# Kernel optimization log

Measured on AMD Instinct MI355X. Metric: run time of the kernel, lower is better.

Reference implementation:

```python
import jax, jax.numpy as jnp
import numpy as np

RES = 192      # resolution
RANK = 8       # low-rank
FD = 32        # feature_dim
NFPD = 32      # num_features_per_dim = round(32768**(1/3))
RADIUS = 1.3
NI = 128       # n_intersections
STEP = 0.0352  # step_size
B = 2048       # rays


def setup_inputs():
    key = jax.random.key(0)
    ks = jax.random.split(key, 12)
    ro = jax.random.normal(ks[0], (B, 3), dtype=jnp.float32)
    ro = ro / jnp.linalg.norm(ro, axis=-1, keepdims=True) * 2.5  # origins outside the cube
    rd = -ro + 0.1 * jax.random.normal(ks[1], (B, 3), dtype=jnp.float32)
    rd = rd / jnp.linalg.norm(rd, axis=-1, keepdims=True)        # roughly toward origin
    def nrm(k, shape, std):
        return std * jax.random.normal(k, shape, dtype=jnp.float32)
    return {
        "rays_o": ro, "rays_d": rd,
        "Gxy": nrm(ks[2], (RES, RES, 3, RANK), 0.1),
        "Gxz": nrm(ks[3], (RES, RES, 3, RANK), 0.1),
        "Gyz": nrm(ks[4], (RES, RES, 3, RANK), 0.1),
        "F_grid": nrm(ks[5], (NFPD, NFPD, NFPD, FD), 0.05),
        "sW0": nrm(ks[6], (FD, 128), FD ** -0.5),
        "sW1": nrm(ks[7], (128, 128), 128 ** -0.5),
        "sW2": nrm(ks[8], (128, 16), 128 ** -0.5),
        "cW0": nrm(ks[9], (31, 64), 31 ** -0.5),
        "cW1": nrm(ks[10], (64, 64), 64 ** -0.5),
        "cW2": nrm(ks[11], (64, 3), 64 ** -0.5),
    }


def trilinear(vol, coords):
    # vol: [D,H,W,C]; coords: [N,3] as (x,y,z) in [-1,1]; x indexes W (last spatial dim)
    # matches torch grid_sample(align_corners=True, mode='bilinear', padding_mode='border')
    D, H, W, C = vol.shape
    def prep(c, size):
        idx = jnp.clip((c + 1.0) * 0.5 * (size - 1), 0.0, size - 1.0)  # border clamp
        i0 = jnp.clip(jnp.floor(idx).astype(jnp.int32), 0, size - 2)
        return i0, i0 + 1, idx - i0
    x0, x1, wx = prep(coords[:, 0], W)
    y0, y1, wy = prep(coords[:, 1], H)
    z0, z1, wz = prep(coords[:, 2], D)
    wx = wx[:, None]; wy = wy[:, None]; wz = wz[:, None]
    def g(zi, yi, xi):
        return vol[zi, yi, xi]  # [N,C]
    c00 = g(z0, y0, x0) * (1 - wx) + g(z0, y0, x1) * wx
    c01 = g(z0, y1, x0) * (1 - wx) + g(z0, y1, x1) * wx
    c10 = g(z1, y0, x0) * (1 - wx) + g(z1, y0, x1) * wx
    c11 = g(z1, y1, x0) * (1 - wx) + g(z1, y1, x1) * wx
    c0 = c00 * (1 - wy) + c01 * wy
    c1 = c10 * (1 - wy) + c11 * wy
    return c0 * (1 - wz) + c1 * wz


def sh16(d):
    # tcnn SphericalHarmonics degree 4 on directions (input (d+1)/2 is unmapped back to d internally)
    x, y, z = d[:, 0], d[:, 1], d[:, 2]
    x2, y2, z2 = x * x, y * y, z * z
    return jnp.stack([
        jnp.full_like(x, 0.28209479177387814),
        -0.48860251190291987 * y,
        0.48860251190291987 * z,
        -0.48860251190291987 * x,
        1.0925484305920792 * x * y,
        -1.0925484305920792 * y * z,
        0.94617469575755997 * z2 - 0.31539156525251999,
        -1.0925484305920792 * x * z,
        0.54627421529603959 * (x2 - y2),
        0.59004358992664352 * y * (-3.0 * x2 + y2),
        2.8906114426405538 * x * y * z,
        0.45704579946446572 * y * (1.0 - 5.0 * z2),
        0.3731763325901154 * z * (5.0 * z2 - 3.0),
        0.45704579946446572 * x * (1.0 - 5.0 * z2),
        1.445305721320277 * z * (x2 - y2),
        0.59004358992664352 * x * (-x2 + 3.0 * y2),
    ], axis=-1)


def _forward(rays_o, rays_d, Gxy, Gxz, Gyz, F_grid, sW0, sW1, sW2, cW0, cW1, cW2):
    b = rays_o.shape[0]
    # --- get_intersections: ray/AABB [-R,R]^3, uniform marching ---
    d = jnp.where(jnp.abs(rays_d) < 1e-9, 1e-9, rays_d)
    t1 = (-RADIUS - rays_o) / d
    t2 = (RADIUS - rays_o) / d
    tmin = jnp.max(jnp.minimum(t1, t2), axis=-1)
    tmax = jnp.min(jnp.maximum(t1, t2), axis=-1)
    near = jnp.maximum(tmin, 0.0)
    ts = near[:, None] + jnp.arange(NI + 1, dtype=jnp.float32) * STEP  # intersections [B,NI+1]
    tmid = 0.5 * (ts[:, :-1] + ts[:, 1:])                              # [B,NI]
    pts = rays_o[:, None, :] + tmid[..., None] * rays_d[:, None, :]    # [B,NI,3]
    mask = (jnp.all(jnp.abs(pts) <= RADIUS, axis=-1)
            & (tmid <= tmax[:, None]) & (tmax > tmin)[:, None])        # [B,NI]
    rdn = rays_d / jnp.linalg.norm(rays_d, axis=-1, keepdims=True)
    # coordinate chain of forward + eval_pts nets out to pts/RADIUS in [-1,1]
    p = ((pts / RADIUS + 1.0) * RES / 2.0) * 2.0 / RES - 1.0
    pf = p.reshape(-1, 3)
    # --- densify low-rank tri-plane grid: sum_r Gxy*Gxz*Gyz -> [RES,RES,RES,3] ---
    grid = jnp.zeros((RES, RES, RES, 3), dtype=Gxy.dtype)
    for r in range(RANK):  # fixed small rank; avoids a [RES^3,3,RANK] intermediate
        grid = grid + (Gxy[:, :, None, :, r] * Gxz[:, None, :, :, r] * Gyz[None, :, :, :, r])
    # --- eval_pts: grid_sample -> hash-feature grid_sample -> MLPs ---
    Gvals = trilinear(grid, pf)            # [N,3]
    Fvals = trilinear(F_grid, Gvals)       # [N,FD]
    h = jax.nn.relu(Fvals @ sW0)
    h = jax.nn.relu(h @ sW1)
    out16 = h @ sW2                        # [N,16]
    sigma = out16[:, 0].reshape(b, NI)
    sigma = jax.nn.relu(jnp.where(mask, sigma, 0.0))
    rdn_pts = jnp.broadcast_to(rdn[:, None, :], (b, NI, 3)).reshape(-1, 3)
    ci = jnp.concatenate([sh16(rdn_pts), out16[:, 1:]], axis=-1)  # [N,31]
    c = jax.nn.relu(ci @ cW0)
    c = jax.nn.relu(c @ cW1)
    color = (c @ cW2).reshape(b, NI, 3)
    color = jnp.where(mask[..., None], color, 0.0)
    # --- sigma2alpha + shrgb2rgb (white background) ---
    dists = ts[:, 1:] - ts[:, :-1]         # |rdn| == 1
    alpha = 1.0 - jnp.exp(-sigma * dists)
    T = jnp.cumprod(1.0 - alpha + 1e-10, axis=-1)
    T = jnp.concatenate([jnp.ones_like(T[:, :1]), T[:, :-1]], axis=-1)  # exclusive
    w = alpha * T                          # abs_light [B,NI]
    rgb = jax.nn.sigmoid(color)
    acc = jnp.sum(w, axis=-1)
    return jnp.sum(w[..., None] * rgb, axis=1) + (1.0 - acc)[..., None]  # [B,3]


def reference(rays_o, rays_d, Gxy, Gxz, Gyz, F_grid, sW0, sW1, sW2, cW0, cW1, cW2):
    return _forward(rays_o, rays_d, Gxy, Gxz, Gyz, F_grid, sW0, sW1, sW2, cW0, cW1, cW2)
```

## Files before the change

kernel.cpp:

```cpp
#include <hip/hip_runtime.h>
#include <math.h>

#define RES 192
#define RANK 8
#define NI 128
#define LW 136

typedef __attribute__((ext_vector_type(8))) _Float16 h8;
typedef __attribute__((ext_vector_type(2))) _Float16 h2f;
typedef __attribute__((ext_vector_type(4))) float floatx4;

#define OFF_SW0 0
#define OFF_SW1 4096
#define OFF_SW2 20480
#define OFF_CW0 22528
#define OFF_CW1 24576
#define OFF_CW2 28672
#define PACK_TOTAL 29696

#define TRI_CELLS (RES*RES)
#define TRI_TOTAL (3*TRI_CELLS*24)
#define FG_TOTAL  (32*32*32*32)
#define PREP_TOTAL (PACK_TOTAL + TRI_TOTAL + FG_TOTAL)

__device__ __forceinline__ void prep_idx(float c, int size, int& i0, float& f){
    float idx = (c + 1.0f)*0.5f*(float)(size-1);
    idx = fminf(fmaxf(idx, 0.0f), (float)(size-1));
    int ii = (int)idx;
    if (ii > size-2) ii = size-2;
    i0 = ii;
    f = idx - (float)ii;
}

__device__ __forceinline__ float wred64(float v){
    #pragma unroll
    for (int o=32;o>0;o>>=1) v += __shfl_down(v, o, 64);
    return v;
}

__device__ __forceinline__ h8 shx1(h8 v){
    union { h8 h; int i[4]; } u; u.h = v;
    #pragma unroll
    for (int k=0;k<4;k++) u.i[k] = __shfl_xor(u.i[k], 1, 64);
    return u.h;
}

__global__ void __launch_bounds__(256) prep_all(
    const float* __restrict__ sW0, const float* __restrict__ sW1,
    const float* __restrict__ sW2, const float* __restrict__ cW0,
    const float* __restrict__ cW1, const float* __restrict__ cW2,
    const float* __restrict__ Gxy, const float* __restrict__ Gxz,
    const float* __restrict__ Gyz, const float* __restrict__ F_grid,
    _Float16* __restrict__ Wp, _Float16* __restrict__ Gp, _Float16* __restrict__ Fg)
{
    int e = blockIdx.x*256 + threadIdx.x;
    if (e < PACK_TOTAL){
        const float* src; int K, N, ksteps, base;
        if      (e < OFF_SW1){ src=sW0; K=32;  N=128; ksteps=1; base=OFF_SW0; }
        else if (e < OFF_SW2){ src=sW1; K=128; N=128; ksteps=4; base=OFF_SW1; }
        else if (e < OFF_CW0){ src=sW2; K=128; N=16;  ksteps=4; base=OFF_SW2; }
        else if (e < OFF_CW1){ src=cW0; K=31;  N=64;  ksteps=1; base=OFF_CW0; }
        else if (e < OFF_CW2){ src=cW1; K=64;  N=64;  ksteps=2; base=OFF_CW1; }
        else                 { src=cW2; K=64;  N=3;   ksteps=2; base=OFF_CW2; }
        int i = e - base;
        int j = i & 7, lane = (i>>3)&63, t = i>>9;
        int ks = t % ksteps, nt = t / ksteps;
        int k = ks*32 + (lane>>4)*8 + j;
        int n = nt*16 + (lane&15);
        float v = (k < K && n < N) ? src[k*N + n] : 0.0f;
        Wp[e] = (_Float16)v;
        return;
    }
    int e2 = e - PACK_TOTAL;
    if (e2 < TRI_TOTAL){
        int p    = e2 / (TRI_CELLS*24);
        int rem  = e2 - p*(TRI_CELLS*24);
        int cell = rem / 24;
        int c    = rem - cell*24;
        const float* src = (p==0) ? Gxy : (p==1) ? Gxz : Gyz;
        Gp[((size_t)(p*TRI_CELLS + cell))*32 + c] = (_Float16)src[(size_t)cell*24 + c];
        return;
    }
    int e3 = e2 - TRI_TOTAL;
    Fg[e3] = (_Float16)F_grid[e3];
}

__launch_bounds__(256, 4)
__global__ void nerf_fused(
    const float* __restrict__ rays_o, const float* __restrict__ rays_d,
    const _Float16* __restrict__ Gp, const _Float16* __restrict__ Fg,
    const _Float16* __restrict__ Wp, float* __restrict__ out)
{
    __shared__ _Float16 buf[128*LW];
    __shared__ float sigmaArr[128];
    __shared__ float rgbArr[128*3];
    __shared__ float wtot[2];
    __shared__ float partial[8];

    const int tid  = threadIdx.x;
    const int lane = tid & 63;
    const int wv   = tid >> 6;
    const int ray  = blockIdx.x;

    const int rowbase = wv*32;
    const int col  = lane & 15;
    const int quad = lane >> 4;
    const int ar0  = rowbase + col;
    const int ar1  = ar0 + 16;

    const float ox = rays_o[ray*3+0], oy = rays_o[ray*3+1], oz = rays_o[ray*3+2];
    const float dx = rays_d[ray*3+0], dy = rays_d[ray*3+1], dz = rays_d[ray*3+2];

    float sdx = (fabsf(dx) < 1e-9f) ? 1e-9f : dx;
    float sdy = (fabsf(dy) < 1e-9f) ? 1e-9f : dy;
    float sdz = (fabsf(dz) < 1e-9f) ? 1e-9f : dz;
    float t1x = (-1.3f - ox)/sdx, t2x = (1.3f - ox)/sdx;
    float t1y = (-1.3f - oy)/sdy, t2y = (1.3f - oy)/sdy;
    float t1z = (-1.3f - oz)/sdz, t2z = (1.3f - oz)/sdz;
    float tmin = fmaxf(fminf(t1x,t2x), fmaxf(fminf(t1y,t2y), fminf(t1z,t2z)));
    float tmax = fminf(fmaxf(t1x,t2x), fminf(fmaxf(t1y,t2y), fmaxf(t1z,t2z)));
    float nearv = fmaxf(tmin, 0.0f);

    bool skipAll;
    {
        int sid = rowbase + (lane & 31);
        float w_ts0 = nearv + (float)sid     * 0.0352f;
        float w_ts1 = nearv + (float)(sid+1) * 0.0352f;
        float w_tm  = 0.5f*(w_ts0+w_ts1);
        float wpx = ox + w_tm*dx, wpy = oy + w_tm*dy, wpz = oz + w_tm*dz;
        bool m = (fabsf(wpx)<=1.3f) && (fabsf(wpy)<=1.3f) && (fabsf(wpz)<=1.3f)
               && (w_tm<=tmax) && (tmax>tmin);
        skipAll = (__ballot(m) == 0ULL);
    }

    if (!skipAll){
        {
            const int s = rowbase + (lane >> 1);
            const int h = lane & 1;

            float ts0 = nearv + (float)s     * 0.0352f;
            float ts1 = nearv + (float)(s+1) * 0.0352f;
            float tmid = 0.5f*(ts0+ts1);
            float px = ox + tmid*dx, py = oy + tmid*dy, pz = oz + tmid*dz;
            bool mask = (fabsf(px)<=1.3f) && (fabsf(py)<=1.3f) && (fabsf(pz)<=1.3f)
                      && (tmid<=tmax) && (tmax>tmin);

            h8 FVa = {0,0,0,0,0,0,0,0};
            h8 FVb = {0,0,0,0,0,0,0,0};

            if (mask){
                float p0 = (px/1.3f + 1.0f)*192.0f/2.0f*2.0f/192.0f - 1.0f;
                float p1 = (py/1.3f + 1.0f)*192.0f/2.0f*2.0f/192.0f - 1.0f;
                float p2 = (pz/1.3f + 1.0f)*192.0f/2.0f*2.0f/192.0f - 1.0f;

                int x0, y0, z0; float fx, fy, fz;
                prep_idx(p0, RES, x0, fx);
                prep_idx(p1, RES, y0, fy);
                prep_idx(p2, RES, z0, fz);

                const int zi  = z0 + h;
                const float wzc = h ? fz : (1.0f - fz);
                const int yiA = y0 + h;
                const int yiB = y0 + 1 - h;

                h8 XYA[3], XYB[3], XZ0[3], XZ1[3], YZo0[3], YZo1[3];
                {
                    const h8* pxyA = (const h8*)(Gp + ((size_t)(zi*RES + yiA))*32);
                    const h8* pxyB = (const h8*)(Gp + ((size_t)(zi*RES + yiB))*32);
                    const h8* px0  = (const h8*)(Gp + ((size_t)(TRI_CELLS + zi*RES + x0  ))*32);
                    const h8* px1  = (const h8*)(Gp + ((size_t)(TRI_CELLS + zi*RES + x0+1))*32);
                    const h8* py0  = (const h8*)(Gp + ((size_t)(2*TRI_CELLS + yiA*RES + x0  ))*32);
                    const h8* py1  = (const h8*)(Gp + ((size_t)(2*TRI_CELLS + yiA*RES + x0+1))*32);
                    #pragma unroll
                    for (int q=0;q<3;q++){
                        XYA[q]=pxyA[q]; XYB[q]=pxyB[q];
                        XZ0[q]=px0[q];  XZ1[q]=px1[q];
                        YZo0[q]=py0[q]; YZo1[q]=py1[q];
                    }
                }
                h8 YZp0[3], YZp1[3];
                #pragma unroll
                for (int q=0;q<3;q++){ YZp0[q]=shx1(YZo0[q]); YZp1[q]=shx1(YZo1[q]); }

                const float wyA = h ? fy : (1.0f - fy);
                const float wyB = h ? (1.0f - fy) : fy;

                h8 ACC0 = {0,0,0,0,0,0,0,0};
                h8 ACC1 = {0,0,0,0,0,0,0,0};
                h8 ACC2 = {0,0,0,0,0,0,0,0};
                #pragma unroll
                for (int yo=0; yo<2; yo++){
                    const float wy = yo ? wyB : wyA;
                    #pragma unroll
                    for (int xc=0; xc<2; xc++){
                        const float wx = xc ? fx : (1.0f - fx);
                        const _Float16 wh = (_Float16)(wzc*wy*wx);
                        const h8 w8 = {wh,wh,wh,wh,wh,wh,wh,wh};
                        h8 Q0, Q1, Q2;
                        if (yo==0){
                            const h8* YZv = xc ? YZo1 : YZo0;
                            Q0 = (XYA[0]*(xc?XZ1[0]:XZ0[0]))*YZv[0];
                            Q1 = (XYA[1]*(xc?XZ1[1]:XZ0[1]))*YZv[1];
                            Q2 = (XYA[2]*(xc?XZ1[2]:XZ0[2]))*YZv[2];
                        } else {
                            const h8* YZv = xc ? YZp1 : YZp0;
                            Q0 = (XYB[0]*(xc?XZ1[0]:XZ0[0]))*YZv[0];
                            Q1 = (XYB[1]*(xc?XZ1[1]:XZ0[1]))*YZv[1];
                            Q2 = (XYB[2]*(xc?XZ1[2]:XZ0[2]))*YZv[2];
                        }
                        ACC0 = __builtin_elementwise_fma(Q0, w8, ACC0);
                        ACC1 = __builtin_elementwise_fma(Q1, w8, ACC1);
                        ACC2 = __builtin_elementwise_fma(Q2, w8, ACC2);
                    }
                }
                h2f a0h = __builtin_shufflevector(ACC0,ACC0,0,1) + __builtin_shufflevector(ACC0,ACC0,2,3);
                h2f b0h = __builtin_shufflevector(ACC0,ACC0,4,5) + __builtin_shufflevector(ACC0,ACC0,6,7);
                h2f c0h = a0h + b0h;
                float gv0 = (float)c0h[0] + (float)c0h[1];
                h2f a1h = __builtin_shufflevector(ACC1,ACC1,0,1) + __builtin_shufflevector(ACC1,ACC1,2,3);
                h2f b1h = __builtin_shufflevector(ACC1,ACC1,4,5) + __builtin_shufflevector(ACC1,ACC1,6,7);
                h2f c1h = a1h + b1h;
                float gv1 = (float)c1h[0] + (float)c1h[1];
                h2f a2h = __builtin_shufflevector(ACC2,ACC2,0,1) + __builtin_shufflevector(ACC2,ACC2,2,3);
                h2f b2h = __builtin_shufflevector(ACC2,ACC2,4,5) + __builtin_shufflevector(ACC2,ACC2,6,7);
                h2f c2h = a2h + b2h;
                float gv2 = (float)c2h[0] + (float)c2h[1];

                gv0 += __shfl_xor(gv0, 1, 64);
                gv1 += __shfl_xor(gv1, 1, 64);
                gv2 += __shfl_xor(gv2, 1, 64);

                int a0,b0,c0; float fa,fb,fc;
                prep_idx(gv2, 32, a0, fa);
                prep_idx(gv1, 32, b0, fb);
                prep_idx(gv0, 32, c0, fc);
                #pragma unroll
                for (int zc=0; zc<2; zc++){
                    const int zi2 = a0+zc; const float wz2 = zc ? fa : 1.f-fa;
                    #pragma unroll
                    for (int yc=0; yc<2; yc++){
                        const int yi2 = b0+yc; const float wy2 = yc ? fb : 1.f-fb;
                        #pragma unroll
                        for (int xc=0; xc<2; xc++){
                            const int xi2 = c0+xc; const float wx2 = xc ? fc : 1.f-fc;
                            const _Float16 wh = (_Float16)(wz2*wy2*wx2);
                            const h8 w8 = {wh,wh,wh,wh,wh,wh,wh,wh};
                            const h8* pf = (const h8*)(Fg + ((size_t)((zi2*32+yi2)*32+xi2))*32 + h*16);
                            FVa = __builtin_elementwise_fma(pf[0], w8, FVa);
                            FVb = __builtin_elementwise_fma(pf[1], w8, FVb);
                        }
                    }
                }
            }

            *(h8*)&buf[s*LW + h*16]     = FVa;
            *(h8*)&buf[s*LW + h*16 + 8] = FVb;
        }

        {
            h8 a0 = *(const h8*)&buf[ar0*LW + quad*8];
            h8 a1 = *(const h8*)&buf[ar1*LW + quad*8];
            const h8* W = (const h8*)(Wp + OFF_SW0);
            #pragma unroll
            for (int nt=0; nt<8; nt++){
                h8 b = W[nt*64 + lane];
                floatx4 c0v = {0.f,0.f,0.f,0.f}, c1v = {0.f,0.f,0.f,0.f};
                c0v = __builtin_amdgcn_mfma_f32_16x16x32_f16(a0, b, c0v, 0,0,0);
                c1v = __builtin_amdgcn_mfma_f32_16x16x32_f16(a1, b, c1v, 0,0,0);
                #pragma unroll
                for (int r=0;r<4;r++){
                    int row0 = rowbase + quad*4 + r;
                    buf[row0*LW      + nt*16 + col] = (_Float16)fmaxf(c0v[r],0.f);
                    buf[(row0+16)*LW + nt*16 + col] = (_Float16)fmaxf(c1v[r],0.f);
                }
            }
        }

        {
            h8 A0[4], A1[4];
            #pragma unroll
            for (int ks=0;ks<4;ks++){
                A0[ks] = *(const h8*)&buf[ar0*LW + ks*32 + quad*8];
                A1[ks] = *(const h8*)&buf[ar1*LW + ks*32 + quad*8];
            }
            const h8* W = (const h8*)(Wp + OFF_SW1);
            #pragma unroll
            for (int nt=0; nt<8; nt++){
                floatx4 c0v = {0.f,0.f,0.f,0.f}, c1v = {0.f,0.f,0.f,0.f};
                #pragma unroll
                for (int ks=0;ks<4;ks++){
                    h8 b = W[(nt*4+ks)*64 + lane];
                    c0v = __builtin_amdgcn_mfma_f32_16x16x32_f16(A0[ks], b, c0v, 0,0,0);
                    c1v = __builtin_amdgcn_mfma_f32_16x16x32_f16(A1[ks], b, c1v, 0,0,0);
                }
                #pragma unroll
                for (int r=0;r<4;r++){
                    int row0 = rowbase + quad*4 + r;
                    buf[row0*LW      + nt*16 + col] = (_Float16)fmaxf(c0v[r],0.f);
                    buf[(row0+16)*LW + nt*16 + col] = (_Float16)fmaxf(c1v[r],0.f);
                }
            }
        }

        {
            h8 A0[4], A1[4];
            #pragma unroll
            for (int ks=0;ks<4;ks++){
                A0[ks] = *(const h8*)&buf[ar0*LW + ks*32 + quad*8];
                A1[ks] = *(const h8*)&buf[ar1*LW + ks*32 + quad*8];
            }
            const h8* W = (const h8*)(Wp + OFF_SW2);
            floatx4 c0v = {0.f,0.f,0.f,0.f}, c1v = {0.f,0.f,0.f,0.f};
            #pragma unroll
            for (int ks=0;ks<4;ks++){
                h8 b = W[ks*64 + lane];
                c0v = __builtin_amdgcn_mfma_f32_16x16x32_f16(A0[ks], b, c0v, 0,0,0);
                c1v = __builtin_amdgcn_mfma_f32_16x16x32_f16(A1[ks], b, c1v, 0,0,0);
            }
            #pragma unroll
            for (int r=0;r<4;r++){
                int row0 = rowbase + quad*4 + r;
                if (col == 0){
                    sigmaArr[row0]    = c0v[r];
                    sigmaArr[row0+16] = c1v[r];
                } else {
                    buf[row0*LW      + 15 + col] = (_Float16)c0v[r];
                    buf[(row0+16)*LW + 15 + col] = (_Float16)c1v[r];
                }
            }
            const float dn = sqrtf(dx*dx+dy*dy+dz*dz);
            const float X = dx/dn, Y = dy/dn, Z = dz/dn;
            const float X2=X*X, Y2=Y*Y, Z2=Z*Z;
            float sh[16];
            sh[0]= 0.28209479177387814f;
            sh[1]=-0.48860251190291987f*Y;
            sh[2]= 0.48860251190291987f*Z;
            sh[3]=-0.48860251190291987f*X;
            sh[4]= 1.0925484305920792f*X*Y;
            sh[5]=-1.0925484305920792f*Y*Z;
            sh[6]= 0.94617469575756f*Z2 - 0.31539156525252f;
            sh[7]=-1.0925484305920792f*X*Z;
            sh[8]= 0.5462742152960396f*(X2-Y2);
            sh[9]= 0.5900435899266435f*Y*(-3.0f*X2+Y2);
            sh[10]=2.890611442640554f*X*Y*Z;
            sh[11]=0.4570457994644657f*Y*(1.0f-5.0f*Z2);
            sh[12]=0.3731763325901154f*Z*(5.0f*Z2-3.0f);
            sh[13]=0.4570457994644657f*X*(1.0f-5.0f*Z2);
            sh[14]=1.445305721320277f*Z*(X2-Y2);
            sh[15]=0.5900435899266435f*X*(-X2+3.0f*Y2);
            if (lane < 32){
                int row = rowbase + lane;
                #pragma unroll
                for (int k=0;k<16;k++) buf[row*LW + k] = (_Float16)sh[k];
            }
        }

        {
            h8 a0 = *(const h8*)&buf[ar0*LW + quad*8];
            h8 a1 = *(const h8*)&buf[ar1*LW + quad*8];
            const h8* W = (const h8*)(Wp + OFF_CW0);
            #pragma unroll
            for (int nt=0; nt<4; nt++){
                h8 b = W[nt*64 + lane];
                floatx4 c0v = {0.f,0.f,0.f,0.f}, c1v = {0.f,0.f,0.f,0.f};
                c0v = __builtin_amdgcn_mfma_f32_16x16x32_f16(a0, b, c0v, 0,0,0);
                c1v = __builtin_amdgcn_mfma_f32_16x16x32_f16(a1, b, c1v, 0,0,0);
                #pragma unroll
                for (int r=0;r<4;r++){
                    int row0 = rowbase + quad*4 + r;
                    buf[row0*LW      + nt*16 + col] = (_Float16)fmaxf(c0v[r],0.f);
                    buf[(row0+16)*LW + nt*16 + col] = (_Float16)fmaxf(c1v[r],0.f);
                }
            }
        }

        {
            h8 A0[2], A1[2];
            #pragma unroll
            for (int ks=0;ks<2;ks++){
                A0[ks] = *(const h8*)&buf[ar0*LW + ks*32 + quad*8];
                A1[ks] = *(const h8*)&buf[ar1*LW + ks*32 + quad*8];
            }
            const h8* W = (const h8*)(Wp + OFF_CW1);
            #pragma unroll
            for (int nt=0; nt<4; nt++){
                floatx4 c0v = {0.f,0.f,0.f,0.f}, c1v = {0.f,0.f,0.f,0.f};
                #pragma unroll
                for (int ks=0;ks<2;ks++){
                    h8 b = W[(nt*2+ks)*64 + lane];
                    c0v = __builtin_amdgcn_mfma_f32_16x16x32_f16(A0[ks], b, c0v, 0,0,0);
                    c1v = __builtin_amdgcn_mfma_f32_16x16x32_f16(A1[ks], b, c1v, 0,0,0);
                }
                #pragma unroll
                for (int r=0;r<4;r++){
                    int row0 = rowbase + quad*4 + r;
                    buf[row0*LW      + nt*16 + col] = (_Float16)fmaxf(c0v[r],0.f);
                    buf[(row0+16)*LW + nt*16 + col] = (_Float16)fmaxf(c1v[r],0.f);
                }
            }
        }

        {
            h8 A0[2], A1[2];
            #pragma unroll
            for (int ks=0;ks<2;ks++){
                A0[ks] = *(const h8*)&buf[ar0*LW + ks*32 + quad*8];
                A1[ks] = *(const h8*)&buf[ar1*LW + ks*32 + quad*8];
            }
            const h8* W = (const h8*)(Wp + OFF_CW2);
            floatx4 c0v = {0.f,0.f,0.f,0.f}, c1v = {0.f,0.f,0.f,0.f};
            #pragma unroll
            for (int ks=0;ks<2;ks++){
                h8 b = W[ks*64 + lane];
                c0v = __builtin_amdgcn_mfma_f32_16x16x32_f16(A0[ks], b, c0v, 0,0,0);
                c1v = __builtin_amdgcn_mfma_f32_16x16x32_f16(A1[ks], b, c1v, 0,0,0);
            }
            if (col < 3){
                #pragma unroll
                for (int r=0;r<4;r++){
                    int row0 = rowbase + quad*4 + r;
                    rgbArr[row0*3 + col]      = c0v[r];
                    rgbArr[(row0+16)*3 + col] = c1v[r];
                }
            }
        }
    }

    __syncthreads();

    {
        float alpha = 0.f, rr = 0.f, rg = 0.f, rb = 0.f;
        if (tid < 128){
            float ts0 = nearv + (float)tid     * 0.0352f;
            float ts1 = nearv + (float)(tid+1) * 0.0352f;
            float tmid = 0.5f*(ts0+ts1);
            float dist = ts1 - ts0;
            float px = ox + tmid*dx, py = oy + tmid*dy, pz = oz + tmid*dz;
            bool mask = (fabsf(px)<=1.3f) && (fabsf(py)<=1.3f) && (fabsf(pz)<=1.3f)
                      && (tmid<=tmax) && (tmax>tmin);
            float sg = mask ? fmaxf(sigmaArr[tid], 0.f) : 0.f;
            alpha = 1.0f - expf(-sg*dist);
            if (mask){
                rr = 1.0f/(1.0f+expf(-rgbArr[tid*3+0]));
                rg = 1.0f/(1.0f+expf(-rgbArr[tid*3+1]));
                rb = 1.0f/(1.0f+expf(-rgbArr[tid*3+2]));
            }
        }
        float p = 1.0f - alpha + 1e-10f;
        #pragma unroll
        for (int off=1; off<64; off<<=1){
            float u = __shfl_up(p, off, 64);
            if (lane >= off) p *= u;
        }
        if (tid < 128 && lane == 63) wtot[wv] = p;
        float excl = __shfl_up(p, 1, 64);
        if (lane == 0) excl = 1.0f;
        __syncthreads();
        if (tid < 128){
            float T = excl;
            if (wv == 1) T *= wtot[0];
            float w = alpha * T;
            float v0 = wred64(w*rr);
            float v1 = wred64(w*rg);
            float v2 = wred64(w*rb);
            float v3 = wred64(w);
            if (lane == 0){
                partial[wv*4+0]=v0; partial[wv*4+1]=v1; partial[wv*4+2]=v2; partial[wv*4+3]=v3;
            }
        }
        __syncthreads();
        if (tid == 0){
            float acc = partial[3] + partial[7];
            float bg  = 1.0f - acc;
            out[ray*3+0] = partial[0] + partial[4] + bg;
            out[ray*3+1] = partial[1] + partial[5] + bg;
            out[ray*3+2] = partial[2] + partial[6] + bg;
        }
    }
}

extern "C" void kernel_launch(void* const* d_in, const int* in_sizes, int n_in,
                              void* d_out, int out_size, void* d_ws, size_t ws_size,
                              hipStream_t stream){
    const float* rays_o = (const float*)d_in[0];
    const float* rays_d = (const float*)d_in[1];
    const float* Gxy    = (const float*)d_in[2];
    const float* Gxz    = (const float*)d_in[3];
    const float* Gyz    = (const float*)d_in[4];
    const float* F_grid = (const float*)d_in[5];
    const float* sW0    = (const float*)d_in[6];
    const float* sW1    = (const float*)d_in[7];
    const float* sW2    = (const float*)d_in[8];
    const float* cW0    = (const float*)d_in[9];
    const float* cW1    = (const float*)d_in[10];
    const float* cW2    = (const float*)d_in[11];

    _Float16* Wp = (_Float16*)d_ws;
    _Float16* Gp = Wp + PACK_TOTAL;
    _Float16* Fg = Gp + (size_t)3*TRI_CELLS*32;

    prep_all<<<PREP_TOTAL/256, 256, 0, stream>>>(sW0,sW1,sW2,cW0,cW1,cW2,
                                                 Gxy,Gxz,Gyz,F_grid, Wp,Gp,Fg);
    nerf_fused<<<2048, 256, 0, stream>>>(rays_o, rays_d, Gp, Fg, Wp, (float*)d_out);
}
```

Before: 130.7 us.

## Transpose MFMA operands for vectorized LDS stores and vectorize prep conversion

Result: no change. 132.4 us (+1.2%).

```diff
diff --git a/kernel.cpp b/kernel.cpp
--- a/kernel.cpp
+++ b/kernel.cpp
@@ -7,6 +7,7 @@
 #define LW 136
 
 typedef __attribute__((ext_vector_type(8))) _Float16 h8;
+typedef __attribute__((ext_vector_type(4))) _Float16 h4;
 typedef __attribute__((ext_vector_type(2))) _Float16 h2f;
 typedef __attribute__((ext_vector_type(4))) float floatx4;
 
@@ -19,9 +20,9 @@
 #define PACK_TOTAL 29696
 
 #define TRI_CELLS (RES*RES)
-#define TRI_TOTAL (3*TRI_CELLS*24)
+#define CELLS3    (3*TRI_CELLS)
 #define FG_TOTAL  (32*32*32*32)
-#define PREP_TOTAL (PACK_TOTAL + TRI_TOTAL + FG_TOTAL)
+#define PREP2_TOTAL (PACK_TOTAL + CELLS3 + FG_TOTAL/8)
 
 __device__ __forceinline__ void prep_idx(float c, int size, int& i0, float& f){
     float idx = (c + 1.0f)*0.5f*(float)(size-1);
@@ -45,7 +46,17 @@
     return u.h;
 }
 
-__global__ void __launch_bounds__(256) prep_all(
+__device__ __forceinline__ void st4r(_Float16* p, floatx4 v){
+    h4 o = {(_Float16)fmaxf(v[0],0.f), (_Float16)fmaxf(v[1],0.f),
+            (_Float16)fmaxf(v[2],0.f), (_Float16)fmaxf(v[3],0.f)};
+    *(h4*)p = o;
+}
+__device__ __forceinline__ void st4n(_Float16* p, floatx4 v){
+    h4 o = {(_Float16)v[0], (_Float16)v[1], (_Float16)v[2], (_Float16)v[3]};
+    *(h4*)p = o;
+}
+
+__global__ void __launch_bounds__(256) prep_all2(
     const float* __restrict__ sW0, const float* __restrict__ sW1,
     const float* __restrict__ sW2, const float* __restrict__ cW0,
     const float* __restrict__ cW1, const float* __restrict__ cW2,
@@ -56,10 +67,11 @@
     int e = blockIdx.x*256 + threadIdx.x;
     if (e < PACK_TOTAL){
         const float* src; int K, N, ksteps, base;
+        bool cw0remap = false;
         if      (e < OFF_SW1){ src=sW0; K=32;  N=128; ksteps=1; base=OFF_SW0; }
         else if (e < OFF_SW2){ src=sW1; K=128; N=128; ksteps=4; base=OFF_SW1; }
         else if (e < OFF_CW0){ src=sW2; K=128; N=16;  ksteps=4; base=OFF_SW2; }
-        else if (e < OFF_CW1){ src=cW0; K=31;  N=64;  ksteps=1; base=OFF_CW0; }
+        else if (e < OFF_CW1){ src=cW0; K=31;  N=64;  ksteps=1; base=OFF_CW0; cw0remap=true; }
         else if (e < OFF_CW2){ src=cW1; K=64;  N=64;  ksteps=2; base=OFF_CW1; }
         else                 { src=cW2; K=64;  N=3;   ksteps=2; base=OFF_CW2; }
         int i = e - base;
@@ -67,22 +79,45 @@
         int ks = t % ksteps, nt = t / ksteps;
         int k = ks*32 + (lane>>4)*8 + j;
         int n = nt*16 + (lane&15);
-        float v = (k < K && n < N) ? src[k*N + n] : 0.0f;
+        float v;
+        if (cw0remap){
+            v = 0.0f;
+            if (k != 16 && n < N){
+                int ksrc = (k < 16) ? k : k-1;
+                v = src[ksrc*N + n];
+            }
+        } else {
+            v = (k < K && n < N) ? src[k*N + n] : 0.0f;
+        }
         Wp[e] = (_Float16)v;
         return;
     }
     int e2 = e - PACK_TOTAL;
-    if (e2 < TRI_TOTAL){
-        int p    = e2 / (TRI_CELLS*24);
-        int rem  = e2 - p*(TRI_CELLS*24);
-        int cell = rem / 24;
-        int c    = rem - cell*24;
-        const float* src = (p==0) ? Gxy : (p==1) ? Gxz : Gyz;
-        Gp[((size_t)(p*TRI_CELLS + cell))*32 + c] = (_Float16)src[(size_t)cell*24 + c];
+    if (e2 < CELLS3){
+        int p, lc;
+        if      (e2 < TRI_CELLS)   { p = 0; lc = e2; }
+        else if (e2 < 2*TRI_CELLS) { p = 1; lc = e2 - TRI_CELLS; }
+        else                       { p = 2; lc = e2 - 2*TRI_CELLS; }
+        const float* src = ((p==0) ? Gxy : (p==1) ? Gxz : Gyz) + (size_t)lc*24;
+        const float4* s4 = (const float4*)src;
+        float4 a = s4[0], b = s4[1], c = s4[2], d = s4[3], ee = s4[4], ff = s4[5];
+        h8 o0 = {(_Float16)a.x,(_Float16)a.y,(_Float16)a.z,(_Float16)a.w,
+                 (_Float16)b.x,(_Float16)b.y,(_Float16)b.z,(_Float16)b.w};
+        h8 o1 = {(_Float16)c.x,(_Float16)c.y,(_Float16)c.z,(_Float16)c.w,
+                 (_Float16)d.x,(_Float16)d.y,(_Float16)d.z,(_Float16)d.w};
+        h8 o2 = {(_Float16)ee.x,(_Float16)ee.y,(_Float16)ee.z,(_Float16)ee.w,
+                 (_Float16)ff.x,(_Float16)ff.y,(_Float16)ff.z,(_Float16)ff.w};
+        h8 zz = {0,0,0,0,0,0,0,0};
+        h8* dst = (h8*)(Gp + (size_t)e2*32);
+        dst[0]=o0; dst[1]=o1; dst[2]=o2; dst[3]=zz;
         return;
     }
-    int e3 = e2 - TRI_TOTAL;
-    Fg[e3] = (_Float16)F_grid[e3];
+    int t = e2 - CELLS3;
+    const float4* s4 = (const float4*)(F_grid + (size_t)t*8);
+    float4 a = s4[0], b = s4[1];
+    h8 o = {(_Float16)a.x,(_Float16)a.y,(_Float16)a.z,(_Float16)a.w,
+            (_Float16)b.x,(_Float16)b.y,(_Float16)b.z,(_Float16)b.w};
+    ((h8*)Fg)[t] = o;
 }
 
 __launch_bounds__(256, 4)
@@ -265,14 +300,10 @@
             for (int nt=0; nt<8; nt++){
                 h8 b = W[nt*64 + lane];
                 floatx4 c0v = {0.f,0.f,0.f,0.f}, c1v = {0.f,0.f,0.f,0.f};
-                c0v = __builtin_amdgcn_mfma_f32_16x16x32_f16(a0, b, c0v, 0,0,0);
-                c1v = __builtin_amdgcn_mfma_f32_16x16x32_f16(a1, b, c1v, 0,0,0);
-                #pragma unroll
-                for (int r=0;r<4;r++){
-                    int row0 = rowbase + quad*4 + r;
-                    buf[row0*LW      + nt*16 + col] = (_Float16)fmaxf(c0v[r],0.f);
-                    buf[(row0+16)*LW + nt*16 + col] = (_Float16)fmaxf(c1v[r],0.f);
-                }
+                c0v = __builtin_amdgcn_mfma_f32_16x16x32_f16(b, a0, c0v, 0,0,0);
+                c1v = __builtin_amdgcn_mfma_f32_16x16x32_f16(b, a1, c1v, 0,0,0);
+                st4r(&buf[ar0*LW + nt*16 + quad*4], c0v);
+                st4r(&buf[ar1*LW + nt*16 + quad*4], c1v);
             }
         }
 
@@ -290,15 +321,11 @@
                 #pragma unroll
                 for (int ks=0;ks<4;ks++){
                     h8 b = W[(nt*4+ks)*64 + lane];
-                    c0v = __builtin_amdgcn_mfma_f32_16x16x32_f16(A0[ks], b, c0v, 0,0,0);
-                    c1v = __builtin_amdgcn_mfma_f32_16x16x32_f16(A1[ks], b, c1v, 0,0,0);
+                    c0v = __builtin_amdgcn_mfma_f32_16x16x32_f16(b, A0[ks], c0v, 0,0,0);
+                    c1v = __builtin_amdgcn_mfma_f32_16x16x32_f16(b, A1[ks], c1v, 0,0,0);
                 }
-                #pragma unroll
-                for (int r=0;r<4;r++){
-                    int row0 = rowbase + quad*4 + r;
-                    buf[row0*LW      + nt*16 + col] = (_Float16)fmaxf(c0v[r],0.f);
-                    buf[(row0+16)*LW + nt*16 + col] = (_Float16)fmaxf(c1v[r],0.f);
-                }
+                st4r(&buf[ar0*LW + nt*16 + quad*4], c0v);
+                st4r(&buf[ar1*LW + nt*16 + quad*4], c1v);
             }
         }
 
@@ -314,19 +341,14 @@
             #pragma unroll
             for (int ks=0;ks<4;ks++){
                 h8 b = W[ks*64 + lane];
-                c0v = __builtin_amdgcn_mfma_f32_16x16x32_f16(A0[ks], b, c0v, 0,0,0);
-                c1v = __builtin_amdgcn_mfma_f32_16x16x32_f16(A1[ks], b, c1v, 0,0,0);
-            }
-            #pragma unroll
-            for (int r=0;r<4;r++){
-                int row0 = rowbase + quad*4 + r;
-                if (col == 0){
-                    sigmaArr[row0]    = c0v[r];
-                    sigmaArr[row0+16] = c1v[r];
-                } else {
-                    buf[row0*LW      + 15 + col] = (_Float16)c0v[r];
-                    buf[(row0+16)*LW + 15 + col] = (_Float16)c1v[r];
-                }
+                c0v = __builtin_amdgcn_mfma_f32_16x16x32_f16(b, A0[ks], c0v, 0,0,0);
+                c1v = __builtin_amdgcn_mfma_f32_16x16x32_f16(b, A1[ks], c1v, 0,0,0);
+            }
+            st4n(&buf[ar0*LW + 16 + quad*4], c0v);
+            st4n(&buf[ar1*LW + 16 + quad*4], c1v);
+            if (quad == 0){
+                sigmaArr[ar0] = c0v[0];
+                sigmaArr[ar1] = c1v[0];
             }
             const float dn = sqrtf(dx*dx+dy*dy+dz*dz);
             const float X = dx/dn, Y = dy/dn, Z = dz/dn;
@@ -363,14 +385,10 @@
             for (int nt=0; nt<4; nt++){
                 h8 b = W[nt*64 + lane];
                 floatx4 c0v = {0.f,0.f,0.f,0.f}, c1v = {0.f,0.f,0.f,0.f};
-                c0v = __builtin_amdgcn_mfma_f32_16x16x32_f16(a0, b, c0v, 0,0,0);
-                c1v = __builtin_amdgcn_mfma_f32_16x16x32_f16(a1, b, c1v, 0,0,0);
-                #pragma unroll
-                for (int r=0;r<4;r++){
-                    int row0 = rowbase + quad*4 + r;
-                    buf[row0*LW      + nt*16 + col] = (_Float16)fmaxf(c0v[r],0.f);
-                    buf[(row0+16)*LW + nt*16 + col] = (_Float16)fmaxf(c1v[r],0.f);
-                }
+                c0v = __builtin_amdgcn_mfma_f32_16x16x32_f16(b, a0, c0v, 0,0,0);
+                c1v = __builtin_amdgcn_mfma_f32_16x16x32_f16(b, a1, c1v, 0,0,0);
+                st4r(&buf[ar0*LW + nt*16 + quad*4], c0v);
+                st4r(&buf[ar1*LW + nt*16 + quad*4], c1v);
             }
         }
 
@@ -388,15 +406,11 @@
                 #pragma unroll
                 for (int ks=0;ks<2;ks++){
                     h8 b = W[(nt*2+ks)*64 + lane];
-                    c0v = __builtin_amdgcn_mfma_f32_16x16x32_f16(A0[ks], b, c0v, 0,0,0);
-                    c1v = __builtin_amdgcn_mfma_f32_16x16x32_f16(A1[ks], b, c1v, 0,0,0);
+                    c0v = __builtin_amdgcn_mfma_f32_16x16x32_f16(b, A0[ks], c0v, 0,0,0);
+                    c1v = __builtin_amdgcn_mfma_f32_16x16x32_f16(b, A1[ks], c1v, 0,0,0);
                 }
-                #pragma unroll
-                for (int r=0;r<4;r++){
-                    int row0 = rowbase + quad*4 + r;
-                    buf[row0*LW      + nt*16 + col] = (_Float16)fmaxf(c0v[r],0.f);
-                    buf[(row0+16)*LW + nt*16 + col] = (_Float16)fmaxf(c1v[r],0.f);
-                }
+                st4r(&buf[ar0*LW + nt*16 + quad*4], c0v);
+                st4r(&buf[ar1*LW + nt*16 + quad*4], c1v);
             }
         }
 
@@ -412,16 +426,16 @@
             #pragma unroll
             for (int ks=0;ks<2;ks++){
                 h8 b = W[ks*64 + lane];
-                c0v = __builtin_amdgcn_mfma_f32_16x16x32_f16(A0[ks], b, c0v, 0,0,0);
-                c1v = __builtin_amdgcn_mfma_f32_16x16x32_f16(A1[ks], b, c1v, 0,0,0);
-            }
-            if (col < 3){
-                #pragma unroll
-                for (int r=0;r<4;r++){
-                    int row0 = rowbase + quad*4 + r;
-                    rgbArr[row0*3 + col]      = c0v[r];
-                    rgbArr[(row0+16)*3 + col] = c1v[r];
-                }
+                c0v = __builtin_amdgcn_mfma_f32_16x16x32_f16(b, A0[ks], c0v, 0,0,0);
+                c1v = __builtin_amdgcn_mfma_f32_16x16x32_f16(b, A1[ks], c1v, 0,0,0);
+            }
+            if (quad == 0){
+                rgbArr[ar0*3+0] = c0v[0];
+                rgbArr[ar0*3+1] = c0v[1];
+                rgbArr[ar0*3+2] = c0v[2];
+                rgbArr[ar1*3+0] = c1v[0];
+                rgbArr[ar1*3+1] = c1v[1];
+                rgbArr[ar1*3+2] = c1v[2];
             }
         }
     }
@@ -499,7 +513,7 @@
     _Float16* Gp = Wp + PACK_TOTAL;
     _Float16* Fg = Gp + (size_t)3*TRI_CELLS*32;
 
-    prep_all<<<PREP_TOTAL/256, 256, 0, stream>>>(sW0,sW1,sW2,cW0,cW1,cW2,
-                                                 Gxy,Gxz,Gyz,F_grid, Wp,Gp,Fg);
+    prep_all2<<<PREP2_TOTAL/256, 256, 0, stream>>>(sW0,sW1,sW2,cW0,cW1,cW2,
+                                                   Gxy,Gxz,Gyz,F_grid, Wp,Gp,Fg);
     nerf_fused<<<2048, 256, 0, stream>>>(rays_o, rays_d, Gp, Fg, Wp, (float*)d_out);
 }
```
